# Optimization experiments

Hardware: AMD Instinct MI355X
Metric: run time of the kernel (lower is better)

Reference implementation:

```python
import jax, jax.numpy as jnp
import numpy as np

DECAY = 0.99
EPS = 1e-05


def setup_inputs() -> dict:
    key = jax.random.key(0)
    k1, k2, k3, k4 = jax.random.split(key, 4)
    B, T, D, V = 8, 2048, 256, 8192
    return {
        "input": jax.random.normal(k1, (B, T, D), dtype=jnp.float32),
        "embed": jax.random.normal(k2, (V, D), dtype=jnp.float32),
        "cluster_size": jax.random.uniform(k3, (V,), dtype=jnp.float32),
        "embed_avg": jax.random.normal(k4, (V, D), dtype=jnp.float32),
    }


def reference(input, embed, cluster_size, embed_avg):
    # input: [B,T,D]; embed: [V,D]
    B, T, D = input.shape
    V = embed.shape[0]
    # squared euclidean distances (argmin identical to cdist argmin)
    d2 = (
        jnp.sum(input * input, axis=-1, keepdims=True)
        - 2.0 * jnp.einsum("btd,vd->btv", input, embed)
        + jnp.sum(embed * embed, axis=-1)
    )  # [B,T,V]
    codes = jnp.argmin(d2, axis=-1)  # [B,T] int
    quantize = jnp.take(embed, codes, axis=0)  # [B,T,D]

    # EMA codebook update (training-mode buffer update, faithful to update_embed)
    flat_codes = codes.reshape(-1)  # [B*T]
    flat_x = input.reshape(-1, D)
    counts = jax.ops.segment_sum(
        jnp.ones_like(flat_codes, dtype=input.dtype), flat_codes, num_segments=V
    )  # onehot.sum(0) over all B*T tokens
    # codebook = mean over T of per-timestep onehot^T @ x == segment_sum / T
    codebook = jax.ops.segment_sum(flat_x, flat_codes, num_segments=V) / T  # [V,D]
    new_cluster_size = cluster_size * DECAY + counts * (1.0 - DECAY)
    new_embed_avg = embed_avg * DECAY + codebook * (1.0 - DECAY)
    new_embed = new_embed_avg / (new_cluster_size + EPS)[:, None]

    # straight-through estimator
    quantize = input + jax.lax.stop_gradient(quantize - input)
    return quantize, codes, new_embed, new_cluster_size, new_embed_avg
```

## Files before the change

kernel.cpp:

```cpp
#include <hip/hip_runtime.h>
#include <math.h>

#define M_TOK 16384
#define DIM   256
#define VOC   8192

#define BM 128
#define BN 128
#define NBLK_N (VOC / BN)
#define GAP_EPS 1.5f

typedef unsigned short u16;
typedef unsigned long long u64;
typedef __attribute__((ext_vector_type(8))) __bf16 bf16x8;
typedef __attribute__((ext_vector_type(4))) float f32x4;

#define WS_ESQ      0
#define WS_CANDV    40960
#define WS_CANDI    1089536
#define WS_CANDS    2138112
#define WS_XHI      3186688
#define WS_EHI      7380992
#define WS_COUNTS   9478144
#define WS_SUMS     9486336
#define WS_ZERO_OFF_BYTES ((size_t)WS_COUNTS * 4)
#define WS_ZERO_BYTES     ((size_t)(8192 + 2097152 + 16) * 4)

#define OUT_Q   0
#define OUT_C   4194304
#define OUT_NE  4210688
#define OUT_NCS 6307840
#define OUT_NEA 6316032

__device__ inline u16 f2bf_rn(float x) {
    unsigned u = __float_as_uint(x);
    unsigned r = u + 0x7FFFu + ((u >> 16) & 1u);
    return (u16)(r >> 16);
}
__device__ inline unsigned f2key(float f) {
    unsigned b = __float_as_uint(f);
    return (b & 0x80000000u) ? ~b : (b | 0x80000000u);
}
__device__ inline float key2f(unsigned k) {
    unsigned b = (k & 0x80000000u) ? (k ^ 0x80000000u) : ~k;
    return __uint_as_float(b);
}

__global__ __launch_bounds__(256) void prep_kernel(
    const float* __restrict__ X, const float* __restrict__ E,
    u16* __restrict__ Xhi, u16* __restrict__ Ehi,
    float* __restrict__ esq)
{
    int row  = blockIdx.x * 4 + (threadIdx.x >> 6);
    int lane = threadIdx.x & 63;
    bool isX = row < M_TOK;
    int r = isX ? row : row - M_TOK;
    const float* src = isX ? X + (size_t)row * DIM : E + (size_t)r * DIM;
    float4 v = ((const float4*)src)[lane];

    ushort4 h;
    h.x = f2bf_rn(v.x); h.y = f2bf_rn(v.y);
    h.z = f2bf_rn(v.z); h.w = f2bf_rn(v.w);
    u16* dh = isX ? Xhi : Ehi;
    *(ushort4*)&dh[(size_t)r * DIM + lane * 4] = h;

    if (!isX) {
        float s = v.x * v.x + v.y * v.y + v.z * v.z + v.w * v.w;
        #pragma unroll
        for (int o = 1; o < 64; o <<= 1) s += __shfl_xor(s, o, 64);
        if (lane == 0) esq[r] = s;
    }
}

__global__ __launch_bounds__(256, 2) void mfma_argmin_kernel(
    const u16* __restrict__ Xhi, const u16* __restrict__ Ehi,
    const float* __restrict__ esq,
    float* __restrict__ candV, int* __restrict__ candI, float* __restrict__ candS)
{
    __shared__ __align__(16) char tiles[4 * 8192];

    const int tid = threadIdx.x;
    const int w = tid >> 6, l = tid & 63;
    const int wy = w >> 1, wx = w & 1;
    const int m0 = blockIdx.x * BM;
    const int n0 = blockIdx.y * BN;

    f32x4 acc[4][4];
    #pragma unroll
    for (int i = 0; i < 4; ++i)
        #pragma unroll
        for (int j = 0; j < 4; ++j) acc[i][j] = (f32x4)0.0f;

    const u16* gbase = (w < 2) ? Xhi : Ehi;
    const int row0   = (w < 2) ? m0 : n0;
    const int koff   = (w & 1) * 32;
    const int swz_c = (l & 3) ^ ((l >> 3) & 3);
    const u16* gsrc0 = gbase + (size_t)(row0 + (l >> 2)) * DIM + koff + swz_c * 8;
    char* ltile = tiles + w * 8192;

    const int frow = l & 15, fq = l >> 4;
    const int fs = ((fq ^ ((frow >> 1) & 3)) * 16);
    const char* a0P = tiles + 0 * 8192 + (wy * 64 + frow) * 64 + fs;
    const char* a1P = tiles + 1 * 8192 + (wy * 64 + frow) * 64 + fs;
    const char* b0P = tiles + 2 * 8192 + (wx * 64 + frow) * 64 + fs;
    const char* b1P = tiles + 3 * 8192 + (wx * 64 + frow) * 64 + fs;

    for (int ks = 0; ks < 4; ++ks) {
        const int k0 = ks * 64;
        __syncthreads();
        #pragma unroll
        for (int i = 0; i < 8; ++i) {
            __builtin_amdgcn_global_load_lds(
                (const __attribute__((address_space(1))) unsigned int*)(gsrc0 + (size_t)i * 16 * DIM + k0),
                (__attribute__((address_space(3))) unsigned int*)(ltile + i * 1024),
                16, 0, 0);
        }
        __syncthreads();

        bf16x8 a0[4], a1[4];
        #pragma unroll
        for (int mt = 0; mt < 4; ++mt) {
            a0[mt] = *(const bf16x8*)(a0P + mt * 1024);
            a1[mt] = *(const bf16x8*)(a1P + mt * 1024);
        }
        #pragma unroll
        for (int nt = 0; nt < 4; ++nt) {
            bf16x8 b0 = *(const bf16x8*)(b0P + nt * 1024);
            bf16x8 b1 = *(const bf16x8*)(b1P + nt * 1024);
            #pragma unroll
            for (int mt = 0; mt < 4; ++mt) {
                acc[mt][nt] = __builtin_amdgcn_mfma_f32_16x16x32_bf16(b0, a0[mt], acc[mt][nt], 0, 0, 0);
                acc[mt][nt] = __builtin_amdgcn_mfma_f32_16x16x32_bf16(b1, a1[mt], acc[mt][nt], 0, 0, 0);
            }
        }
    }

    __syncthreads();
    float* smB = (float*)tiles;
    int*   smI = (int*)(tiles + 1024);
    float* smS = (float*)(tiles + 2048);

    float eqv[16];
    #pragma unroll
    for (int nt = 0; nt < 4; ++nt) {
        float4 t = *(const float4*)&esq[n0 + wx * 64 + nt * 16 + fq * 4];
        eqv[nt * 4 + 0] = t.x; eqv[nt * 4 + 1] = t.y;
        eqv[nt * 4 + 2] = t.z; eqv[nt * 4 + 3] = t.w;
    }

    #pragma unroll
    for (int mt = 0; mt < 4; ++mt) {
        float b = 3.4e38f, s = 3.4e38f;
        int bi = 0;
        #pragma unroll
        for (int nt = 0; nt < 4; ++nt) {
            #pragma unroll
            for (int r = 0; r < 4; ++r) {
                float v = fmaf(-2.0f, acc[mt][nt][r], eqv[nt * 4 + r]);
                int c = n0 + wx * 64 + nt * 16 + fq * 4 + r;
                if (v < b) { s = b; b = v; bi = c; }
                else if (v < s) s = v;
            }
        }
        #pragma unroll
        for (int o = 16; o < 64; o <<= 1) {
            float ob = __shfl_xor(b, o, 64);
            int   oi = __shfl_xor(bi, o, 64);
            float os = __shfl_xor(s, o, 64);
            bool take = (ob < b) || (ob == b && oi < bi);
            float keep = take ? b : ob;
            b  = take ? ob : b;
            bi = take ? oi : bi;
            s  = fminf(fminf(s, os), keep);
        }
        if (l < 16) {
            int m_loc = wy * 64 + mt * 16 + l;
            smB[wx * 128 + m_loc] = b;
            smI[wx * 128 + m_loc] = bi;
            smS[wx * 128 + m_loc] = s;
        }
    }
    __syncthreads();
    if (tid < 128) {
        float b0 = smB[tid],       b1 = smB[128 + tid];
        int   i0 = smI[tid],       i1 = smI[128 + tid];
        float s0 = smS[tid],       s1 = smS[128 + tid];
        bool take = (b1 < b0);
        float b = take ? b1 : b0;
        int  bi = take ? i1 : i0;
        float s = fminf(fminf(s0, s1), take ? b0 : b1);
        size_t e = (size_t)(m0 + tid) * NBLK_N + blockIdx.y;
        candV[e] = b; candI[e] = bi; candS[e] = s;
    }
}

__global__ __launch_bounds__(256) void post_kernel(
    const float* __restrict__ X, const float* __restrict__ E,
    const float* __restrict__ esq,
    const float* __restrict__ candV, const int* __restrict__ candI,
    const float* __restrict__ candS,
    float* __restrict__ out_q, float* __restrict__ out_codes,
    float* __restrict__ counts, float* __restrict__ sums)
{
    const int lane = threadIdx.x & 63;
    const int row  = blockIdx.x * 4 + (threadIdx.x >> 6);

    float bv = candV[(size_t)row * NBLK_N + lane];
    float bs = candS[(size_t)row * NBLK_N + lane];
    int   bi = candI[(size_t)row * NBLK_N + lane];

    u64 pk = ((u64)f2key(bv) << 32) | (unsigned)bi;
    u64 m = pk;
    #pragma unroll
    for (int o = 1; o < 64; o <<= 1) {
        u64 other = __shfl_xor(m, o, 64);
        m = (other < m) ? other : m;
    }
    float best = key2f((unsigned)(m >> 32));
    int   code = (int)(unsigned)(m & 0xFFFFFFFFull);

    float sec = (pk == m) ? bs : bv;
    #pragma unroll
    for (int o = 1; o < 64; o <<= 1) sec = fminf(sec, __shfl_xor(sec, o, 64));

    const float4 x4 = ((const float4*)&X[(size_t)row * DIM])[lane];

    if (sec - best < GAP_EPS) {
        const float bound = best + GAP_EPS;
        float bestV = 3.4e38f;
        int   bestI = 0x7FFFFFFF;
        u64 mask = __ballot(bv < bound);
        while (mask) {
            int src = __ffsll((unsigned long long)mask) - 1;
            mask &= mask - 1;
            int c = __shfl(bi, src, 64);
            float4 e4 = ((const float4*)&E[(size_t)c * DIM])[lane];
            float d = x4.x * e4.x + x4.y * e4.y + x4.z * e4.z + x4.w * e4.w;
            #pragma unroll
            for (int o = 1; o < 64; o <<= 1) d += __shfl_xor(d, o, 64);
            float v = fmaf(-2.0f, d, esq[c]);
            if (v < bestV || (v == bestV && c < bestI)) { bestV = v; bestI = c; }
        }
        u64 dmask = __ballot(bs < bound);
        while (dmask) {
            int e = __ffsll((unsigned long long)dmask) - 1;
            dmask &= dmask - 1;
            const int c0 = e * BN;
            for (int j = 0; j < BN; j += 4) {
                float4 e0 = ((const float4*)&E[(size_t)(c0 + j + 0) * DIM])[lane];
                float4 e1 = ((const float4*)&E[(size_t)(c0 + j + 1) * DIM])[lane];
                float4 e2 = ((const float4*)&E[(size_t)(c0 + j + 2) * DIM])[lane];
                float4 e3 = ((const float4*)&E[(size_t)(c0 + j + 3) * DIM])[lane];
                float d0 = x4.x * e0.x + x4.y * e0.y + x4.z * e0.z + x4.w * e0.w;
                float d1 = x4.x * e1.x + x4.y * e1.y + x4.z * e1.z + x4.w * e1.w;
                float d2 = x4.x * e2.x + x4.y * e2.y + x4.z * e2.z + x4.w * e2.w;
                float d3 = x4.x * e3.x + x4.y * e3.y + x4.z * e3.z + x4.w * e3.w;
                #pragma unroll
                for (int o = 1; o < 64; o <<= 1) {
                    d0 += __shfl_xor(d0, o, 64);
                    d1 += __shfl_xor(d1, o, 64);
                    d2 += __shfl_xor(d2, o, 64);
                    d3 += __shfl_xor(d3, o, 64);
                }
                float v0 = fmaf(-2.0f, d0, esq[c0 + j + 0]);
                float v1 = fmaf(-2.0f, d1, esq[c0 + j + 1]);
                float v2 = fmaf(-2.0f, d2, esq[c0 + j + 2]);
                float v3 = fmaf(-2.0f, d3, esq[c0 + j + 3]);
                if (v0 < bestV || (v0 == bestV && c0 + j + 0 < bestI)) { bestV = v0; bestI = c0 + j + 0; }
                if (v1 < bestV || (v1 == bestV && c0 + j + 1 < bestI)) { bestV = v1; bestI = c0 + j + 1; }
                if (v2 < bestV || (v2 == bestV && c0 + j + 2 < bestI)) { bestV = v2; bestI = c0 + j + 2; }
                if (v3 < bestV || (v3 == bestV && c0 + j + 3 < bestI)) { bestV = v3; bestI = c0 + j + 3; }
            }
        }
        code = bestI;
    }

    if (lane == 0) {
        out_codes[row] = (float)code;
        atomicAdd(&counts[code], 1.0f);
    }
    float4 e4 = ((const float4*)&E[(size_t)code * DIM])[lane];
    float4 q;
    q.x = x4.x + (e4.x - x4.x);
    q.y = x4.y + (e4.y - x4.y);
    q.z = x4.z + (e4.z - x4.z);
    q.w = x4.w + (e4.w - x4.w);
    ((float4*)&out_q[(size_t)row * DIM])[lane] = q;
    float* s = &sums[(size_t)code * DIM + lane * 4];
    atomicAdd(s + 0, x4.x);
    atomicAdd(s + 1, x4.y);
    atomicAdd(s + 2, x4.z);
    atomicAdd(s + 3, x4.w);
}

__global__ __launch_bounds__(256) void finalize_kernel(
    const float* __restrict__ cs, const float* __restrict__ ea,
    const float* __restrict__ counts, const float* __restrict__ sums,
    float* __restrict__ out_embed, float* __restrict__ out_cs,
    float* __restrict__ out_ea)
{
    int vd = blockIdx.x * 256 + threadIdx.x;
    int v = vd >> 8, d = vd & 255;
    float cnt = counts[v];
    float ncs = cs[v] * 0.99f + cnt * 0.01f;
    float cb  = sums[vd] * (1.0f / 2048.0f);
    float nea = ea[vd] * 0.99f + cb * 0.01f;
    out_ea[vd] = nea;
    out_embed[vd] = nea / (ncs + 1e-5f);
    if (d == 0) out_cs[v] = ncs;
}

extern "C" void kernel_launch(void* const* d_in, const int* in_sizes, int n_in,
                              void* d_out, int out_size, void* d_ws, size_t ws_size,
                              hipStream_t stream)
{
    const float* input     = (const float*)d_in[0];
    const float* embed     = (const float*)d_in[1];
    const float* cluster   = (const float*)d_in[2];
    const float* embed_avg = (const float*)d_in[3];

    float* out = (float*)d_out;
    float* ws  = (float*)d_ws;

    float* esq      = ws + WS_ESQ;
    float* candV    = ws + WS_CANDV;
    int*   candI    = (int*)(ws + WS_CANDI);
    float* candS    = ws + WS_CANDS;
    u16*   Xhi      = (u16*)(ws + WS_XHI);
    u16*   Ehi      = (u16*)(ws + WS_EHI);
    float* counts   = ws + WS_COUNTS;
    float* sums     = ws + WS_SUMS;

    hipMemsetAsync((char*)d_ws + WS_ZERO_OFF_BYTES, 0, WS_ZERO_BYTES, stream);

    prep_kernel<<<(M_TOK + VOC) / 4, 256, 0, stream>>>(
        input, embed, Xhi, Ehi, esq);

    dim3 g1(M_TOK / BM, VOC / BN);
    mfma_argmin_kernel<<<g1, 256, 0, stream>>>(
        Xhi, Ehi, esq, candV, candI, candS);

    post_kernel<<<M_TOK / 4, 256, 0, stream>>>(
        input, embed, esq, candV, candI, candS,
        out + OUT_Q, out + OUT_C, counts, sums);

    finalize_kernel<<<(VOC * DIM) / 256, 256, 0, stream>>>(
        cluster, embed_avg, counts, sums,
        out + OUT_NE, out + OUT_NCS, out + OUT_NEA);
}
```

Before: 301.9 us.

## Replace atomic scatter-add codebook update with counting-sort gather reduction

Removes the global float atomics for counts and per-code sums, along with the workspace memset. A new single-block kernel counting-sorts token indices by code, and finalize then gathers and sums each code's rows directly. The candidate buffers are also packed (value key plus index as one u64) and transposed to a column-major layout, and each post_kernel wave now handles four rows. The cost is an extra serial single-block launch, and finalize load is skewed by cluster-size imbalance.

```diff
diff --git a/kernel.cpp b/kernel.cpp
--- a/kernel.cpp
+++ b/kernel.cpp
@@ -16,15 +16,12 @@
 typedef __attribute__((ext_vector_type(4))) float f32x4;
 
 #define WS_ESQ      0
-#define WS_CANDV    40960
-#define WS_CANDI    1089536
+#define WS_CANDPK   40960
 #define WS_CANDS    2138112
 #define WS_XHI      3186688
-#define WS_EHI      7380992
-#define WS_COUNTS   9478144
-#define WS_SUMS     9486336
-#define WS_ZERO_OFF_BYTES ((size_t)WS_COUNTS * 4)
-#define WS_ZERO_BYTES     ((size_t)(8192 + 2097152 + 16) * 4)
+#define WS_EHI      5283840
+#define WS_OFF      6332416
+#define WS_ROWLIST  6340864
 
 #define OUT_Q   0
 #define OUT_C   4194304
@@ -75,7 +72,7 @@
 __global__ __launch_bounds__(256, 2) void mfma_argmin_kernel(
     const u16* __restrict__ Xhi, const u16* __restrict__ Ehi,
     const float* __restrict__ esq,
-    float* __restrict__ candV, int* __restrict__ candI, float* __restrict__ candS)
+    u64* __restrict__ candPK, float* __restrict__ candS)
 {
     __shared__ __align__(16) char tiles[4 * 8192];
 
@@ -189,125 +186,193 @@
         float b = take ? b1 : b0;
         int  bi = take ? i1 : i0;
         float s = fminf(fminf(s0, s1), take ? b0 : b1);
-        size_t e = (size_t)(m0 + tid) * NBLK_N + blockIdx.y;
-        candV[e] = b; candI[e] = bi; candS[e] = s;
+        size_t e = (size_t)blockIdx.y * M_TOK + (m0 + tid);
+        candPK[e] = ((u64)f2key(b) << 32) | (unsigned)bi;
+        candS[e]  = s;
     }
 }
 
 __global__ __launch_bounds__(256) void post_kernel(
     const float* __restrict__ X, const float* __restrict__ E,
     const float* __restrict__ esq,
-    const float* __restrict__ candV, const int* __restrict__ candI,
-    const float* __restrict__ candS,
-    float* __restrict__ out_q, float* __restrict__ out_codes,
-    float* __restrict__ counts, float* __restrict__ sums)
+    const u64* __restrict__ candPK, const float* __restrict__ candS,
+    float* __restrict__ out_q, float* __restrict__ out_codes)
 {
     const int lane = threadIdx.x & 63;
-    const int row  = blockIdx.x * 4 + (threadIdx.x >> 6);
-
-    float bv = candV[(size_t)row * NBLK_N + lane];
-    float bs = candS[(size_t)row * NBLK_N + lane];
-    int   bi = candI[(size_t)row * NBLK_N + lane];
-
-    u64 pk = ((u64)f2key(bv) << 32) | (unsigned)bi;
-    u64 m = pk;
+    const int wv   = threadIdx.x >> 6;
+    const int row0 = blockIdx.x * 16 + wv * 4;
+
+    for (int rr = 0; rr < 4; ++rr) {
+        const int row = row0 + rr;
+        u64   pk = candPK[(size_t)lane * M_TOK + row];
+        float bs = candS[(size_t)lane * M_TOK + row];
+        float bv = key2f((unsigned)(pk >> 32));
+
+        u64 m = pk;
+        #pragma unroll
+        for (int o = 1; o < 64; o <<= 1) {
+            u64 other = __shfl_xor(m, o, 64);
+            m = (other < m) ? other : m;
+        }
+        float best = key2f((unsigned)(m >> 32));
+        int   code = (int)(unsigned)(m & 0xFFFFFFFFull);
+
+        float sec = (pk == m) ? bs : bv;
+        #pragma unroll
+        for (int o = 1; o < 64; o <<= 1) sec = fminf(sec, __shfl_xor(sec, o, 64));
+
+        const float4 x4 = ((const float4*)&X[(size_t)row * DIM])[lane];
+
+        if (sec - best < GAP_EPS) {
+            const float bound = best + GAP_EPS;
+            float bestV = 3.4e38f;
+            int   bestI = 0x7FFFFFFF;
+            int   bi = (int)(unsigned)(pk & 0xFFFFFFFFull);
+            u64 mask = __ballot(bv < bound);
+            while (mask) {
+                int src = __ffsll((unsigned long long)mask) - 1;
+                mask &= mask - 1;
+                int c = __shfl(bi, src, 64);
+                float4 e4 = ((const float4*)&E[(size_t)c * DIM])[lane];
+                float d = x4.x * e4.x + x4.y * e4.y + x4.z * e4.z + x4.w * e4.w;
+                #pragma unroll
+                for (int o = 1; o < 64; o <<= 1) d += __shfl_xor(d, o, 64);
+                float v = fmaf(-2.0f, d, esq[c]);
+                if (v < bestV || (v == bestV && c < bestI)) { bestV = v; bestI = c; }
+            }
+            u64 dmask = __ballot(bs < bound);
+            while (dmask) {
+                int e = __ffsll((unsigned long long)dmask) - 1;
+                dmask &= dmask - 1;
+                const int c0 = e * BN;
+                for (int j = 0; j < BN; j += 4) {
+                    float4 e0 = ((const float4*)&E[(size_t)(c0 + j + 0) * DIM])[lane];
+                    float4 e1 = ((const float4*)&E[(size_t)(c0 + j + 1) * DIM])[lane];
+                    float4 e2 = ((const float4*)&E[(size_t)(c0 + j + 2) * DIM])[lane];
+                    float4 e3 = ((const float4*)&E[(size_t)(c0 + j + 3) * DIM])[lane];
+                    float d0 = x4.x * e0.x + x4.y * e0.y + x4.z * e0.z + x4.w * e0.w;
+                    float d1 = x4.x * e1.x + x4.y * e1.y + x4.z * e1.z + x4.w * e1.w;
+                    float d2 = x4.x * e2.x + x4.y * e2.y + x4.z * e2.z + x4.w * e2.w;
+                    float d3 = x4.x * e3.x + x4.y * e3.y + x4.z * e3.z + x4.w * e3.w;
+                    #pragma unroll
+                    for (int o = 1; o < 64; o <<= 1) {
+                        d0 += __shfl_xor(d0, o, 64);
+                        d1 += __shfl_xor(d1, o, 64);
+                        d2 += __shfl_xor(d2, o, 64);
+                        d3 += __shfl_xor(d3, o, 64);
+                    }
+                    float v0 = fmaf(-2.0f, d0, esq[c0 + j + 0]);
+                    float v1 = fmaf(-2.0f, d1, esq[c0 + j + 1]);
+                    float v2 = fmaf(-2.0f, d2, esq[c0 + j + 2]);
+                    float v3 = fmaf(-2.0f, d3, esq[c0 + j + 3]);
+                    if (v0 < bestV || (v0 == bestV && c0 + j + 0 < bestI)) { bestV = v0; bestI = c0 + j + 0; }
+                    if (v1 < bestV || (v1 == bestV && c0 + j + 1 < bestI)) { bestV = v1; bestI = c0 + j + 1; }
+                    if (v2 < bestV || (v2 == bestV && c0 + j + 2 < bestI)) { bestV = v2; bestI = c0 + j + 2; }
+                    if (v3 < bestV || (v3 == bestV && c0 + j + 3 < bestI)) { bestV = v3; bestI = c0 + j + 3; }
+                }
+            }
+            code = bestI;
+        }
+
+        if (lane == 0) out_codes[row] = (float)code;
+        float4 e4 = ((const float4*)&E[(size_t)code * DIM])[lane];
+        float4 q;
+        q.x = x4.x + (e4.x - x4.x);
+        q.y = x4.y + (e4.y - x4.y);
+        q.z = x4.z + (e4.z - x4.z);
+        q.w = x4.w + (e4.w - x4.w);
+        ((float4*)&out_q[(size_t)row * DIM])[lane] = q;
+    }
+}
+
+__global__ __launch_bounds__(1024) void buildidx_kernel(
+    const float* __restrict__ codesf,
+    int* __restrict__ off_g, int* __restrict__ rowlist)
+{
+    __shared__ int cnt[VOC];
+    __shared__ int cur[VOC];
+    __shared__ int wtot[16], wbase[16];
+    const int tid = threadIdx.x;
+    const int lane = tid & 63, wid = tid >> 6;
+
+    #pragma unroll
+    for (int i = 0; i < VOC / 1024; ++i) cnt[i * 1024 + tid] = 0;
+    __syncthreads();
+
+    int mycodes[16];
+    #pragma unroll
+    for (int j = 0; j < 16; ++j) {
+        mycodes[j] = (int)codesf[j * 1024 + tid];
+        atomicAdd(&cnt[mycodes[j]], 1);
+    }
+    __syncthreads();
+
+    const int base = tid * 8;
+    int pre[8]; int s = 0;
+    #pragma unroll
+    for (int j = 0; j < 8; ++j) { pre[j] = s; s += cnt[base + j]; }
+    int incl = s;
     #pragma unroll
     for (int o = 1; o < 64; o <<= 1) {
-        u64 other = __shfl_xor(m, o, 64);
-        m = (other < m) ? other : m;
-    }
-    float best = key2f((unsigned)(m >> 32));
-    int   code = (int)(unsigned)(m & 0xFFFFFFFFull);
-
-    float sec = (pk == m) ? bs : bv;
-    #pragma unroll
-    for (int o = 1; o < 64; o <<= 1) sec = fminf(sec, __shfl_xor(sec, o, 64));
-
-    const float4 x4 = ((const float4*)&X[(size_t)row * DIM])[lane];
-
-    if (sec - best < GAP_EPS) {
-        const float bound = best + GAP_EPS;
-        float bestV = 3.4e38f;
-        int   bestI = 0x7FFFFFFF;
-        u64 mask = __ballot(bv < bound);
-        while (mask) {
-            int src = __ffsll((unsigned long long)mask) - 1;
-            mask &= mask - 1;
-            int c = __shfl(bi, src, 64);
-            float4 e4 = ((const float4*)&E[(size_t)c * DIM])[lane];
-            float d = x4.x * e4.x + x4.y * e4.y + x4.z * e4.z + x4.w * e4.w;
-            #pragma unroll
-            for (int o = 1; o < 64; o <<= 1) d += __shfl_xor(d, o, 64);
-            float v = fmaf(-2.0f, d, esq[c]);
-            if (v < bestV || (v == bestV && c < bestI)) { bestV = v; bestI = c; }
-        }
-        u64 dmask = __ballot(bs < bound);
-        while (dmask) {
-            int e = __ffsll((unsigned long long)dmask) - 1;
-            dmask &= dmask - 1;
-            const int c0 = e * BN;
-            for (int j = 0; j < BN; j += 4) {
-                float4 e0 = ((const float4*)&E[(size_t)(c0 + j + 0) * DIM])[lane];
-                float4 e1 = ((const float4*)&E[(size_t)(c0 + j + 1) * DIM])[lane];
-                float4 e2 = ((const float4*)&E[(size_t)(c0 + j + 2) * DIM])[lane];
-                float4 e3 = ((const float4*)&E[(size_t)(c0 + j + 3) * DIM])[lane];
-                float d0 = x4.x * e0.x + x4.y * e0.y + x4.z * e0.z + x4.w * e0.w;
-                float d1 = x4.x * e1.x + x4.y * e1.y + x4.z * e1.z + x4.w * e1.w;
-                float d2 = x4.x * e2.x + x4.y * e2.y + x4.z * e2.z + x4.w * e2.w;
-                float d3 = x4.x * e3.x + x4.y * e3.y + x4.z * e3.z + x4.w * e3.w;
-                #pragma unroll
-                for (int o = 1; o < 64; o <<= 1) {
-                    d0 += __shfl_xor(d0, o, 64);
-                    d1 += __shfl_xor(d1, o, 64);
-                    d2 += __shfl_xor(d2, o, 64);
-                    d3 += __shfl_xor(d3, o, 64);
-                }
-                float v0 = fmaf(-2.0f, d0, esq[c0 + j + 0]);
-                float v1 = fmaf(-2.0f, d1, esq[c0 + j + 1]);
-                float v2 = fmaf(-2.0f, d2, esq[c0 + j + 2]);
-                float v3 = fmaf(-2.0f, d3, esq[c0 + j + 3]);
-                if (v0 < bestV || (v0 == bestV && c0 + j + 0 < bestI)) { bestV = v0; bestI = c0 + j + 0; }
-                if (v1 < bestV || (v1 == bestV && c0 + j + 1 < bestI)) { bestV = v1; bestI = c0 + j + 1; }
-                if (v2 < bestV || (v2 == bestV && c0 + j + 2 < bestI)) { bestV = v2; bestI = c0 + j + 2; }
-                if (v3 < bestV || (v3 == bestV && c0 + j + 3 < bestI)) { bestV = v3; bestI = c0 + j + 3; }
-            }
-        }
-        code = bestI;
-    }
-
-    if (lane == 0) {
-        out_codes[row] = (float)code;
-        atomicAdd(&counts[code], 1.0f);
-    }
-    float4 e4 = ((const float4*)&E[(size_t)code * DIM])[lane];
-    float4 q;
-    q.x = x4.x + (e4.x - x4.x);
-    q.y = x4.y + (e4.y - x4.y);
-    q.z = x4.z + (e4.z - x4.z);
-    q.w = x4.w + (e4.w - x4.w);
-    ((float4*)&out_q[(size_t)row * DIM])[lane] = q;
-    float* s = &sums[(size_t)code * DIM + lane * 4];
-    atomicAdd(s + 0, x4.x);
-    atomicAdd(s + 1, x4.y);
-    atomicAdd(s + 2, x4.z);
-    atomicAdd(s + 3, x4.w);
+        int t = __shfl_up(incl, o, 64);
+        if (lane >= o) incl += t;
+    }
+    if (lane == 63) wtot[wid] = incl;
+    __syncthreads();
+    if (tid == 0) {
+        int a = 0;
+        for (int w2 = 0; w2 < 16; ++w2) { wbase[w2] = a; a += wtot[w2]; }
+    }
+    __syncthreads();
+    const int gb = wbase[wid] + (incl - s);
+    #pragma unroll
+    for (int j = 0; j < 8; ++j) {
+        int o = gb + pre[j];
+        cur[base + j] = o;
+        off_g[base + j] = o;
+    }
+    if (tid == 0) off_g[VOC] = M_TOK;
+    __syncthreads();
+
+    #pragma unroll
+    for (int j = 0; j < 16; ++j) {
+        int p = atomicAdd(&cur[mycodes[j]], 1);
+        rowlist[p] = j * 1024 + tid;
+    }
 }
 
 __global__ __launch_bounds__(256) void finalize_kernel(
+    const float* __restrict__ X,
     const float* __restrict__ cs, const float* __restrict__ ea,
-    const float* __restrict__ counts, const float* __restrict__ sums,
+    const int* __restrict__ off, const int* __restrict__ rowlist,
     float* __restrict__ out_embed, float* __restrict__ out_cs,
     float* __restrict__ out_ea)
 {
-    int vd = blockIdx.x * 256 + threadIdx.x;
-    int v = vd >> 8, d = vd & 255;
-    float cnt = counts[v];
-    float ncs = cs[v] * 0.99f + cnt * 0.01f;
-    float cb  = sums[vd] * (1.0f / 2048.0f);
-    float nea = ea[vd] * 0.99f + cb * 0.01f;
-    out_ea[vd] = nea;
-    out_embed[vd] = nea / (ncs + 1e-5f);
-    if (d == 0) out_cs[v] = ncs;
+    const int lane = threadIdx.x & 63;
+    const int v = blockIdx.x * 4 + (threadIdx.x >> 6);
+    const int o0 = off[v], o1 = off[v + 1];
+
+    float4 acc = {0.0f, 0.0f, 0.0f, 0.0f};
+    for (int i = o0; i < o1; ++i) {
+        int r = rowlist[i];
+        float4 x4 = ((const float4*)&X[(size_t)r * DIM])[lane];
+        acc.x += x4.x; acc.y += x4.y; acc.z += x4.z; acc.w += x4.w;
+    }
+    const float cntv = (float)(o1 - o0);
+    const float ncs = cs[v] * 0.99f + cntv * 0.01f;
+    const float sc = 0.01f / 2048.0f;
+    float4 ea4 = ((const float4*)&ea[(size_t)v * DIM])[lane];
+    float4 nea, oe;
+    nea.x = ea4.x * 0.99f + acc.x * sc;
+    nea.y = ea4.y * 0.99f + acc.y * sc;
+    nea.z = ea4.z * 0.99f + acc.z * sc;
+    nea.w = ea4.w * 0.99f + acc.w * sc;
+    const float den = ncs + 1e-5f;
+    oe.x = nea.x / den; oe.y = nea.y / den;
+    oe.z = nea.z / den; oe.w = nea.w / den;
+    ((float4*)&out_ea[(size_t)v * DIM])[lane] = nea;
+    ((float4*)&out_embed[(size_t)v * DIM])[lane] = oe;
+    if (lane == 0) out_cs[v] = ncs;
 }
 
 extern "C" void kernel_launch(void* const* d_in, const int* in_sizes, int n_in,
@@ -323,28 +388,28 @@
     float* ws  = (float*)d_ws;
 
     float* esq      = ws + WS_ESQ;
-    float* candV    = ws + WS_CANDV;
-    int*   candI    = (int*)(ws + WS_CANDI);
+    u64*   candPK   = (u64*)(ws + WS_CANDPK);
     float* candS    = ws + WS_CANDS;
     u16*   Xhi      = (u16*)(ws + WS_XHI);
     u16*   Ehi      = (u16*)(ws + WS_EHI);
-    float* counts   = ws + WS_COUNTS;
-    float* sums     = ws + WS_SUMS;
-
-    hipMemsetAsync((char*)d_ws + WS_ZERO_OFF_BYTES, 0, WS_ZERO_BYTES, stream);
+    int*   off      = (int*)(ws + WS_OFF);
+    int*   rowlist  = (int*)(ws + WS_ROWLIST);
 
     prep_kernel<<<(M_TOK + VOC) / 4, 256, 0, stream>>>(
         input, embed, Xhi, Ehi, esq);
 
     dim3 g1(M_TOK / BM, VOC / BN);
     mfma_argmin_kernel<<<g1, 256, 0, stream>>>(
-        Xhi, Ehi, esq, candV, candI, candS);
-
-    post_kernel<<<M_TOK / 4, 256, 0, stream>>>(
-        input, embed, esq, candV, candI, candS,
-        out + OUT_Q, out + OUT_C, counts, sums);
-
-    finalize_kernel<<<(VOC * DIM) / 256, 256, 0, stream>>>(
-        cluster, embed_avg, counts, sums,
+        Xhi, Ehi, esq, candPK, candS);
+
+    post_kernel<<<M_TOK / 16, 256, 0, stream>>>(
+        input, embed, esq, candPK, candS,
+        out + OUT_Q, out + OUT_C);
+
+    buildidx_kernel<<<1, 1024, 0, stream>>>(
+        out + OUT_C, off, rowlist);
+
+    finalize_kernel<<<VOC / 4, 256, 0, stream>>>(
+        input, cluster, embed_avg, off, rowlist,
         out + OUT_NE, out + OUT_NCS, out + OUT_NEA);
 }
```

Measured after the change: 318.3 us. +5.4%, slower.

## Pack argmin candidates, transpose candidate layout, fold workspace zeroing into prep

Applied to the files above, without the earlier changes.

The argmin kernel now writes each candidate's key and index as one packed 64-bit value, stored in a block-major layout so consecutive threads write consecutive rows. The post kernel stages the candidates for its four rows through shared memory before doing the wave reductions. The separate memset of the counts and sums workspace is dropped, and prep_kernel zeroes that region instead. This removes one launch and an extra array write, in exchange for a shared-memory transpose step and a barrier in the post kernel.

```diff
diff --git a/kernel.cpp b/kernel.cpp
--- a/kernel.cpp
+++ b/kernel.cpp
@@ -16,15 +16,13 @@
 typedef __attribute__((ext_vector_type(4))) float f32x4;
 
 #define WS_ESQ      0
-#define WS_CANDV    40960
-#define WS_CANDI    1089536
+#define WS_CANDPK   40960
 #define WS_CANDS    2138112
 #define WS_XHI      3186688
-#define WS_EHI      7380992
-#define WS_COUNTS   9478144
-#define WS_SUMS     9486336
-#define WS_ZERO_OFF_BYTES ((size_t)WS_COUNTS * 4)
-#define WS_ZERO_BYTES     ((size_t)(8192 + 2097152 + 16) * 4)
+#define WS_EHI      5283840
+#define WS_COUNTS   6332416
+#define WS_SUMS     6340608
+#define ZERO_F4     526336
 
 #define OUT_Q   0
 #define OUT_C   4194304
@@ -49,7 +47,7 @@
 __global__ __launch_bounds__(256) void prep_kernel(
     const float* __restrict__ X, const float* __restrict__ E,
     u16* __restrict__ Xhi, u16* __restrict__ Ehi,
-    float* __restrict__ esq)
+    float* __restrict__ esq, float4* __restrict__ zbase)
 {
     int row  = blockIdx.x * 4 + (threadIdx.x >> 6);
     int lane = threadIdx.x & 63;
@@ -70,12 +68,18 @@
         for (int o = 1; o < 64; o <<= 1) s += __shfl_xor(s, o, 64);
         if (lane == 0) esq[r] = s;
     }
+
+    int gid = blockIdx.x * 256 + threadIdx.x;
+    if (gid < ZERO_F4) {
+        float4 z = {0.0f, 0.0f, 0.0f, 0.0f};
+        zbase[gid] = z;
+    }
 }
 
 __global__ __launch_bounds__(256, 2) void mfma_argmin_kernel(
     const u16* __restrict__ Xhi, const u16* __restrict__ Ehi,
     const float* __restrict__ esq,
-    float* __restrict__ candV, int* __restrict__ candI, float* __restrict__ candS)
+    u64* __restrict__ candPK, float* __restrict__ candS)
 {
     __shared__ __align__(16) char tiles[4 * 8192];
 
@@ -189,27 +193,37 @@
         float b = take ? b1 : b0;
         int  bi = take ? i1 : i0;
         float s = fminf(fminf(s0, s1), take ? b0 : b1);
-        size_t e = (size_t)(m0 + tid) * NBLK_N + blockIdx.y;
-        candV[e] = b; candI[e] = bi; candS[e] = s;
+        size_t e = (size_t)blockIdx.y * M_TOK + (m0 + tid);
+        candPK[e] = ((u64)f2key(b) << 32) | (unsigned)bi;
+        candS[e]  = s;
     }
 }
 
 __global__ __launch_bounds__(256) void post_kernel(
     const float* __restrict__ X, const float* __restrict__ E,
     const float* __restrict__ esq,
-    const float* __restrict__ candV, const int* __restrict__ candI,
-    const float* __restrict__ candS,
+    const u64* __restrict__ candPK, const float* __restrict__ candS,
     float* __restrict__ out_q, float* __restrict__ out_codes,
     float* __restrict__ counts, float* __restrict__ sums)
 {
+    __shared__ u64   pkS[4][64];
+    __shared__ float sS[4][64];
     const int lane = threadIdx.x & 63;
-    const int row  = blockIdx.x * 4 + (threadIdx.x >> 6);
-
-    float bv = candV[(size_t)row * NBLK_N + lane];
-    float bs = candS[(size_t)row * NBLK_N + lane];
-    int   bi = candI[(size_t)row * NBLK_N + lane];
-
-    u64 pk = ((u64)f2key(bv) << 32) | (unsigned)bi;
+    const int wv   = threadIdx.x >> 6;
+    const int row0 = blockIdx.x * 4;
+
+    {
+        const int e = threadIdx.x >> 2, rr = threadIdx.x & 3;
+        pkS[rr][e] = candPK[(size_t)e * M_TOK + row0 + rr];
+        sS[rr][e]  = candS [(size_t)e * M_TOK + row0 + rr];
+    }
+    __syncthreads();
+
+    const int row = row0 + wv;
+    u64   pk = pkS[wv][lane];
+    float bs = sS[wv][lane];
+    float bv = key2f((unsigned)(pk >> 32));
+
     u64 m = pk;
     #pragma unroll
     for (int o = 1; o < 64; o <<= 1) {
@@ -229,6 +243,7 @@
         const float bound = best + GAP_EPS;
         float bestV = 3.4e38f;
         int   bestI = 0x7FFFFFFF;
+        int   bi = (int)(unsigned)(pk & 0xFFFFFFFFull);
         u64 mask = __ballot(bv < bound);
         while (mask) {
             int src = __ffsll((unsigned long long)mask) - 1;
@@ -323,25 +338,22 @@
     float* ws  = (float*)d_ws;
 
     float* esq      = ws + WS_ESQ;
-    float* candV    = ws + WS_CANDV;
-    int*   candI    = (int*)(ws + WS_CANDI);
+    u64*   candPK   = (u64*)(ws + WS_CANDPK);
     float* candS    = ws + WS_CANDS;
     u16*   Xhi      = (u16*)(ws + WS_XHI);
     u16*   Ehi      = (u16*)(ws + WS_EHI);
     float* counts   = ws + WS_COUNTS;
     float* sums     = ws + WS_SUMS;
 
-    hipMemsetAsync((char*)d_ws + WS_ZERO_OFF_BYTES, 0, WS_ZERO_BYTES, stream);
-
     prep_kernel<<<(M_TOK + VOC) / 4, 256, 0, stream>>>(
-        input, embed, Xhi, Ehi, esq);
+        input, embed, Xhi, Ehi, esq, (float4*)counts);
 
     dim3 g1(M_TOK / BM, VOC / BN);
     mfma_argmin_kernel<<<g1, 256, 0, stream>>>(
-        Xhi, Ehi, esq, candV, candI, candS);
+        Xhi, Ehi, esq, candPK, candS);
 
     post_kernel<<<M_TOK / 4, 256, 0, stream>>>(
-        input, embed, esq, candV, candI, candS,
+        input, embed, esq, candPK, candS,
         out + OUT_Q, out + OUT_C, counts, sums);
 
     finalize_kernel<<<(VOC * DIM) / 256, 256, 0, stream>>>(
```

Result: faster. 295.0 us (-2.3%).
